# Optimization experiments

Measured on AMD Instinct MI355X. Metric: run time of the kernel, lower is better.

Reference implementation:

```python
import jax, jax.numpy as jnp
import numpy as np

HEADS = 8
DIM_HEAD = 64
SCALE = DIM_HEAD ** -0.5


def setup_inputs() -> dict:
    key = jax.random.key(0)
    k1, k2, k3 = jax.random.split(key, 3)
    B, N, D = 4, 2048, HEADS * DIM_HEAD  # D = inner_dim = 512
    x = jax.random.normal(k1, (B, N, D), dtype=jnp.float32)
    # nn.Linear weights stored transposed vs torch; here we use [in, out]
    w_qkv = jax.random.normal(k2, (D, 3 * D), dtype=jnp.float32) * (D ** -0.5)
    w_out = jax.random.normal(k3, (D, D), dtype=jnp.float32) * (D ** -0.5)
    b_out = jnp.zeros((D,), dtype=jnp.float32)
    return {"x": x, "w_qkv": w_qkv, "w_out": w_out, "b_out": b_out}


def reference(x, w_qkv, w_out, b_out):
    B, N, D = x.shape
    qkv = x @ w_qkv  # [B, N, 3D]
    q, k, v = jnp.split(qkv, 3, axis=-1)

    def to_heads(t):  # b n (h d) -> b h n d
        return t.reshape(B, N, HEADS, DIM_HEAD).transpose(0, 2, 1, 3)

    q, k, v = to_heads(q), to_heads(k), to_heads(v)
    dots = jnp.einsum('bhnd,bhmd->bhnm', q, k) * SCALE  # [B,H,N,N]
    attn = jax.nn.softmax(dots, axis=-1)
    out = jnp.einsum('bhnm,bhmd->bhnd', attn, v)  # [B,H,N,d]
    out = out.transpose(0, 2, 1, 3).reshape(B, N, D)  # b h n d -> b n (h d)
    return out @ w_out + b_out
```

## Files before the change

### kernel.cpp

```cpp
#include <hip/hip_runtime.h>

typedef __bf16 bf16;
typedef __bf16 bf16x8 __attribute__((ext_vector_type(8)));
typedef __bf16 bf16x4 __attribute__((ext_vector_type(4)));
typedef float f32x4 __attribute__((ext_vector_type(4)));
typedef float f32x16 __attribute__((ext_vector_type(16)));
typedef unsigned int uint2v __attribute__((ext_vector_type(2)));

#define MFMA16(a, b, c) __builtin_amdgcn_mfma_f32_16x16x32_bf16(a, b, c, 0, 0, 0)
#define MFMA32(a, b, c) __builtin_amdgcn_mfma_f32_32x32x16_bf16(a, b, c, 0, 0, 0)

#define CS 0.18033688011112042f

#if __has_builtin(__builtin_amdgcn_exp2f)
#define EXP2(x) __builtin_amdgcn_exp2f(x)
#else
#define EXP2(x) exp2f(x)
#endif

#define WAIT_VM0() __builtin_amdgcn_s_waitcnt(0x0F70)
#define WAIT_VM8() __builtin_amdgcn_s_waitcnt(0x0F78)

__device__ __forceinline__ void load_lds16(const bf16* g, bf16* l) {
    __builtin_amdgcn_global_load_lds(
        (const __attribute__((address_space(1))) unsigned int*)g,
        (__attribute__((address_space(3))) unsigned int*)l, 16, 0, 0);
}

#if __has_builtin(__builtin_amdgcn_permlane32_swap)
__device__ __forceinline__ bf16x8 build_bfrag(bf16x4 plo, bf16x4 phi, int ) {
    union { bf16x4 b; unsigned int i[2]; } ul, uh;
    ul.b = plo; uh.b = phi;
    uint2v r0 = __builtin_amdgcn_permlane32_swap(ul.i[0], uh.i[0], false, false);
    uint2v r1 = __builtin_amdgcn_permlane32_swap(ul.i[1], uh.i[1], false, false);
    union { unsigned int i[4]; bf16x8 b; } ub;
    ub.i[0] = r0[0]; ub.i[1] = r1[0]; ub.i[2] = r0[1]; ub.i[3] = r1[1];
    return ub.b;
}

__device__ __forceinline__ float sum_halves(float x) {
    union { float f; unsigned int u; } a; a.f = x;
    uint2v r = __builtin_amdgcn_permlane32_swap(a.u, a.u, false, false);
    union { unsigned int u; float f; } b0, b1;
    b0.u = r[0]; b1.u = r[1];
    return b0.f + b1.f;
}
#else
__device__ __forceinline__ bf16x4 shfl_xor32_b64(bf16x4 v) {
    union { bf16x4 b; int i[2]; } u;
    u.b = v;
    u.i[0] = __shfl_xor(u.i[0], 32, 64);
    u.i[1] = __shfl_xor(u.i[1], 32, 64);
    return u.b;
}
__device__ __forceinline__ bf16x8 build_bfrag(bf16x4 plo, bf16x4 phi, int h) {
    bf16x4 xlo = shfl_xor32_b64(plo);
    bf16x4 xhi = shfl_xor32_b64(phi);
    bf16x4 lo4 = h ? xhi : plo;
    bf16x4 hi4 = h ? phi : xlo;
    bf16x8 bb;
#pragma unroll
    for (int i = 0; i < 4; ++i) { bb[i] = lo4[i]; bb[4 + i] = hi4[i]; }
    return bb;
}
__device__ __forceinline__ float sum_halves(float x) {
    return x + __shfl_xor(x, 32, 64);
}
#endif

__global__ __launch_bounds__(256) void f32_to_bf16_kernel(const float* __restrict__ in,
                                                          bf16* __restrict__ out, int n) {
    int i = (blockIdx.x * 256 + threadIdx.x) * 4;
    if (i < n) {
        float4 v = *(const float4*)&in[i];
        bf16x4 o = {(bf16)v.x, (bf16)v.y, (bf16)v.z, (bf16)v.w};
        *(bf16x4*)&out[i] = o;
    }
}

__global__ __launch_bounds__(256) void transpose_f2b(const float* __restrict__ in,
                                                     bf16* __restrict__ out,
                                                     int R, int C) {
    __shared__ float tile[32][33];
    int tx = threadIdx.x & 31, ty = threadIdx.x >> 5;
    int c0 = blockIdx.x * 32, r0 = blockIdx.y * 32;
#pragma unroll
    for (int i = ty; i < 32; i += 8)
        tile[i][tx] = in[(size_t)(r0 + i) * C + c0 + tx];
    __syncthreads();
#pragma unroll
    for (int i = ty; i < 32; i += 8)
        out[(size_t)(c0 + i) * R + r0 + tx] = (bf16)tile[tx][i];
}

__global__ __launch_bounds__(256) void transpose_v_kernel(const bf16* __restrict__ qkv,
                                                          bf16* __restrict__ vt) {
    __shared__ bf16 tile[32][33];
    int tx = threadIdx.x & 31, ty = threadIdx.x >> 5;
    int bh = blockIdx.z, b = bh >> 3, h = bh & 7;
    int n0 = blockIdx.x * 32, d0 = blockIdx.y * 32;
#pragma unroll
    for (int i = ty; i < 32; i += 8)
        tile[i][tx] = qkv[(size_t)(b * 2048 + n0 + i) * 1536 + 1024 + h * 64 + d0 + tx];
    __syncthreads();
#pragma unroll
    for (int i = ty; i < 32; i += 8)
        vt[(size_t)(bh * 64 + d0 + i) * 2048 + n0 + tx] = tile[tx][i];
}

template <int MT, int MODE, typename OutT>
__global__ __launch_bounds__(256, (MT == 4) ? 2 : 4)
void gemm_bt_kernel(const bf16* __restrict__ A,
                    const bf16* __restrict__ Bt,
                    const float* __restrict__ bias,
                    OutT* __restrict__ C,
                    int M, int N, int K) {
    const int BM = MT * 32;
    __shared__ bf16 As[BM * 64];
    __shared__ bf16 Bs[128 * 64];
    int t = threadIdx.x;
    int lane = t & 63, w = t >> 6;
    int wr = w >> 1, wc = w & 1;
    int quad = lane >> 4, r16 = lane & 15;
    int m0 = blockIdx.y * BM, n0 = blockIdx.x * 128;

    const f32x4 fzero = {0.f, 0.f, 0.f, 0.f};
    f32x4 acc[MT][4];
#pragma unroll
    for (int i = 0; i < MT; ++i)
#pragma unroll
        for (int j = 0; j < 4; ++j) acc[i][j] = fzero;

    const bf16* ap[MT]; bf16* ad[MT];
    const bf16* bp[4];  bf16* bd[4];
#pragma unroll
    for (int i = 0; i < MT; ++i) {
        int ci = i * 256 + t;
        int row = ci >> 3, cp = ci & 7, cc = cp ^ (row & 7);
        ap[i] = &A[(size_t)(m0 + row) * K + cc * 8];
        ad[i] = &As[ci * 8];
    }
#pragma unroll
    for (int i = 0; i < 4; ++i) {
        int ci = i * 256 + t;
        int row = ci >> 3, cp = ci & 7, cc = cp ^ (row & 7);
        bp[i] = &Bt[(size_t)(n0 + row) * K + cc * 8];
        bd[i] = &Bs[ci * 8];
    }

    for (int k0 = 0; k0 < K; k0 += 64) {
        __syncthreads();
#pragma unroll
        for (int i = 0; i < MT; ++i) { load_lds16(ap[i], ad[i]); ap[i] += 64; }
#pragma unroll
        for (int i = 0; i < 4; ++i) { load_lds16(bp[i], bd[i]); bp[i] += 64; }
        __syncthreads();
#pragma unroll
        for (int ks = 0; ks < 2; ++ks) {
            bf16x8 af[MT], bfr[4];
            int cp = (ks * 4 + quad) ^ (r16 & 7);
#pragma unroll
            for (int mt = 0; mt < MT; ++mt)
                af[mt] = *(const bf16x8*)&As[(wr * (BM / 2) + mt * 16 + r16) * 64 + cp * 8];
#pragma unroll
            for (int nt = 0; nt < 4; ++nt)
                bfr[nt] = *(const bf16x8*)&Bs[(wc * 64 + nt * 16 + r16) * 64 + cp * 8];
#pragma unroll
            for (int mt = 0; mt < MT; ++mt)
#pragma unroll
                for (int nt = 0; nt < 4; ++nt)
                    acc[mt][nt] = MFMA16(af[mt], bfr[nt], acc[mt][nt]);
        }
    }
#pragma unroll
    for (int mt = 0; mt < MT; ++mt)
#pragma unroll
        for (int nt = 0; nt < 4; ++nt)
#pragma unroll
            for (int r = 0; r < 4; ++r) {
                int row = m0 + wr * (BM / 2) + mt * 16 + quad * 4 + r;
                int col = n0 + wc * 64 + nt * 16 + r16;
                float v = acc[mt][nt][r];
                if (MODE == 1 && n0 < 512) v *= CS;
                if (MODE == 2) v += bias[col];
                C[(size_t)row * N + col] = (OutT)v;
            }
}

__global__ __launch_bounds__(128, 2) void attn_kernel(const bf16* __restrict__ qkv,
                                                      const bf16* __restrict__ vt,
                                                      bf16* __restrict__ out) {
    __shared__ __align__(16) char smemraw[32768];
    bf16* stage = (bf16*)smemraw;

    int t = threadIdx.x;
    int lane = t & 63, w = t >> 6;
    int h = lane >> 5, q = lane & 31;
    int bh = blockIdx.y, b = bh >> 3, hd = bh & 7;
    int qb = blockIdx.x * 64;

    bf16x8 qf[2][4];
#pragma unroll
    for (int sub = 0; sub < 2; ++sub) {
        size_t qoff = (size_t)(b * 2048 + qb + sub * 32 + q) * 1536 + hd * 64;
#pragma unroll
        for (int s = 0; s < 4; ++s)
            qf[sub][s] = *(const bf16x8*)&qkv[qoff + s * 16 + h * 8];
    }

    f32x16 o_acc[2][2];
#pragma unroll
    for (int sub = 0; sub < 2; ++sub)
#pragma unroll
        for (int db = 0; db < 2; ++db)
#pragma unroll
            for (int i = 0; i < 16; ++i) o_acc[sub][db][i] = 0.f;
    float psum[2] = {0.f, 0.f};

    bf16* base = stage + w * 8192;

    const bf16* kp[4]; const bf16* vp[4];
    int kdo[4], vdo[4];
#pragma unroll
    for (int rdd = 0; rdd < 4; ++rdd) {
        int ciK = rdd * 64 + lane;
        int rowK = ciK >> 3, ccK = (ciK & 7) ^ (rowK & 7);
        kp[rdd] = &qkv[(size_t)(b * 2048 + w * 1024 + rowK) * 1536 + 512 + hd * 64 + ccK * 8];
        kdo[rdd] = ciK * 8;
        int ciV = rdd * 64 + lane;
        int rowV = ciV >> 2, ccV = (ciV & 3) ^ (rowV & 3);
        vp[rdd] = &vt[(size_t)(bh * 64 + rowV) * 2048 + w * 1024 + ccV * 8];
        vdo[rdd] = 2048 + ciV * 8;
    }

#pragma unroll
    for (int rdd = 0; rdd < 4; ++rdd) {
        load_lds16(kp[rdd], base + kdo[rdd]);  kp[rdd] += (size_t)32 * 1536;
        load_lds16(vp[rdd], base + vdo[rdd]);  vp[rdd] += 32;
    }

    for (int it = 0; it < 32; ++it) {
        const bf16* Ks = base + (it & 1) * 4096;
        const bf16* Vs = Ks + 2048;
        if (it < 31) {
            bf16* nb = base + ((it + 1) & 1) * 4096;
#pragma unroll
            for (int rdd = 0; rdd < 4; ++rdd) {
                load_lds16(kp[rdd], nb + kdo[rdd]);  kp[rdd] += (size_t)32 * 1536;
                load_lds16(vp[rdd], nb + vdo[rdd]);  vp[rdd] += 32;
            }
            WAIT_VM8();
        } else {
            WAIT_VM0();
        }

        bf16x8 kf[4];
#pragma unroll
        for (int s = 0; s < 4; ++s) {
            int cp = (s * 2 + h) ^ (q & 7);
            kf[s] = *(const bf16x8*)&Ks[q * 64 + cp * 8];
        }
        bf16x8 vf[2][2];
#pragma unroll
        for (int kstep = 0; kstep < 2; ++kstep)
#pragma unroll
            for (int db = 0; db < 2; ++db) {
                int cp = (kstep * 2 + h) ^ (q & 3);
                vf[kstep][db] = *(const bf16x8*)&Vs[(db * 32 + q) * 32 + cp * 8];
            }

#pragma unroll
        for (int sub = 0; sub < 2; ++sub) {
            f32x16 sacc;
#pragma unroll
            for (int i = 0; i < 16; ++i) sacc[i] = 0.f;
#pragma unroll
            for (int s = 0; s < 4; ++s)
                sacc = MFMA32(kf[s], qf[sub][s], sacc);

            bf16x4 pk[4];
            float ps0 = 0.f, ps1 = 0.f, ps2 = 0.f, ps3 = 0.f;
#pragma unroll
            for (int i = 0; i < 4; ++i) {
                float p0 = EXP2(sacc[i]);
                float p1 = EXP2(sacc[4 + i]);
                float p2 = EXP2(sacc[8 + i]);
                float p3 = EXP2(sacc[12 + i]);
                ps0 += p0; ps1 += p1; ps2 += p2; ps3 += p3;
                pk[0][i] = (bf16)p0; pk[1][i] = (bf16)p1;
                pk[2][i] = (bf16)p2; pk[3][i] = (bf16)p3;
            }
            psum[sub] += (ps0 + ps1) + (ps2 + ps3);
            bf16x8 bfr0 = build_bfrag(pk[0], pk[1], h);
            bf16x8 bfr1 = build_bfrag(pk[2], pk[3], h);

#pragma unroll
            for (int db = 0; db < 2; ++db) {
                o_acc[sub][db] = MFMA32(vf[0][db], bfr0, o_acc[sub][db]);
                o_acc[sub][db] = MFMA32(vf[1][db], bfr1, o_acc[sub][db]);
            }
        }
    }

    float l_own[2];
#pragma unroll
    for (int sub = 0; sub < 2; ++sub)
        l_own[sub] = sum_halves(psum[sub]);

    __syncthreads();
    float* Of = (float*)smemraw;
    float* Lf = (float*)(smemraw + 17408);

    if (w == 1) {
#pragma unroll
        for (int sub = 0; sub < 2; ++sub) {
#pragma unroll
            for (int db = 0; db < 2; ++db)
#pragma unroll
                for (int r = 0; r < 16; ++r) {
                    int d = db * 32 + (r & 3) + 8 * (r >> 2) + 4 * h;
                    Of[(sub * 32 + q) * 68 + d] = o_acc[sub][db][r];
                }
            if (h == 0) Lf[sub * 32 + q] = l_own[sub];
        }
    }
    __syncthreads();
    if (w == 0) {
#pragma unroll
        for (int sub = 0; sub < 2; ++sub) {
#pragma unroll
            for (int db = 0; db < 2; ++db)
#pragma unroll
                for (int r = 0; r < 16; ++r) {
                    int d = db * 32 + (r & 3) + 8 * (r >> 2) + 4 * h;
                    Of[(sub * 32 + q) * 68 + d] += o_acc[sub][db][r];
                }
            if (h == 0) Lf[sub * 32 + q] += l_own[sub];
        }
    }
    __syncthreads();

    {
        int row = t >> 1, half = t & 1;
        float linv = 1.f / Lf[row];
        const float* src = &Of[row * 68 + half * 32];
        bf16* dst = &out[(size_t)(b * 2048 + qb + row) * 512 + hd * 64 + half * 32];
#pragma unroll
        for (int i = 0; i < 4; ++i) {
            f32x4 a = *(const f32x4*)&src[i * 8];
            f32x4 c = *(const f32x4*)&src[i * 8 + 4];
            bf16x8 o8;
#pragma unroll
            for (int j = 0; j < 4; ++j) {
                o8[j] = (bf16)(a[j] * linv);
                o8[4 + j] = (bf16)(c[j] * linv);
            }
            *(bf16x8*)&dst[i * 8] = o8;
        }
    }
}

extern "C" void kernel_launch(void* const* d_in, const int* in_sizes, int n_in,
                              void* d_out, int out_size, void* d_ws, size_t ws_size,
                              hipStream_t stream) {
    const float* x     = (const float*)d_in[0];
    const float* w_qkv = (const float*)d_in[1];
    const float* w_out = (const float*)d_in[2];
    const float* b_out = (const float*)d_in[3];
    float* out = (float*)d_out;

    char* ws = (char*)d_ws;
    size_t off = 0;
    bf16* xb    = (bf16*)(ws + off); off += (size_t)8192 * 512 * 2;
    bf16* wqkvT = (bf16*)(ws + off); off += (size_t)1536 * 512 * 2;
    bf16* woutT = (bf16*)(ws + off); off += (size_t)512 * 512 * 2;
    bf16* qkv   = (bf16*)(ws + off); off += (size_t)8192 * 1536 * 2;
    bf16* vt    = (bf16*)(ws + off); off += (size_t)32 * 64 * 2048 * 2;
    bf16* attn  = (bf16*)(ws + off);

    f32_to_bf16_kernel<<<4096, 256, 0, stream>>>(x, xb, 8192 * 512);
    transpose_f2b<<<dim3(48, 16), 256, 0, stream>>>(w_qkv, wqkvT, 512, 1536);
    transpose_f2b<<<dim3(16, 16), 256, 0, stream>>>(w_out, woutT, 512, 512);
    gemm_bt_kernel<4, 1, bf16><<<dim3(12, 64), 256, 0, stream>>>(
        xb, wqkvT, nullptr, qkv, 8192, 1536, 512);
    transpose_v_kernel<<<dim3(64, 2, 32), 256, 0, stream>>>(qkv, vt);
    attn_kernel<<<dim3(32, 32), 128, 0, stream>>>(qkv, vt, attn);
    gemm_bt_kernel<2, 2, float><<<dim3(4, 128), 256, 0, stream>>>(
        attn, woutT, b_out, out, 8192, 512, 512);
}
```

Before: 164.4 us.

## Double-buffer GEMM LDS tiles and remap block indices for XCD locality

Double-buffers the GEMM shared-memory A/B tiles so the next K-slice's global-to-LDS loads are issued before computing the current slice. Waits use partial vmcnt counts with raw barriers. Both the GEMM and attention kernels remap linear block IDs so consecutive tiles land on the same XCD (stride-8 interleave), aiming for better L2 reuse. The extra LDS lowers the GEMM occupancy hint from 4 to 3 blocks for the smaller tile variant.

```diff
diff --git a/kernel.cpp b/kernel.cpp
--- a/kernel.cpp
+++ b/kernel.cpp
@@ -19,7 +19,11 @@
 #endif
 
 #define WAIT_VM0() __builtin_amdgcn_s_waitcnt(0x0F70)
+#define WAIT_VM6() __builtin_amdgcn_s_waitcnt(0x0F76)
 #define WAIT_VM8() __builtin_amdgcn_s_waitcnt(0x0F78)
+
+#define BARRIER() __builtin_amdgcn_s_barrier()
+#define CFENCE() asm volatile("" ::: "memory")
 
 __device__ __forceinline__ void load_lds16(const bf16* g, bf16* l) {
     __builtin_amdgcn_global_load_lds(
@@ -109,20 +113,26 @@
 }
 
 template <int MT, int MODE, typename OutT>
-__global__ __launch_bounds__(256, (MT == 4) ? 2 : 4)
+__global__ __launch_bounds__(256, (MT == 4) ? 2 : 3)
 void gemm_bt_kernel(const bf16* __restrict__ A,
                     const bf16* __restrict__ Bt,
                     const float* __restrict__ bias,
                     OutT* __restrict__ C,
                     int M, int N, int K) {
     const int BM = MT * 32;
-    __shared__ bf16 As[BM * 64];
-    __shared__ bf16 Bs[128 * 64];
+    const int ASZ = BM * 64, BSZ = 128 * 64;
+    __shared__ bf16 As[2 * ASZ];
+    __shared__ bf16 Bs[2 * BSZ];
     int t = threadIdx.x;
     int lane = t & 63, w = t >> 6;
     int wr = w >> 1, wc = w & 1;
     int quad = lane >> 4, r16 = lane & 15;
-    int m0 = blockIdx.y * BM, n0 = blockIdx.x * 128;
+
+    int lin = blockIdx.y * gridDim.x + blockIdx.x;
+    int cpx = (gridDim.x * gridDim.y) >> 3;
+    int nl = (lin & 7) * cpx + (lin >> 3);
+    int bx = nl % gridDim.x, by = nl / gridDim.x;
+    int m0 = by * BM, n0 = bx * 128;
 
     const f32x4 fzero = {0.f, 0.f, 0.f, 0.f};
     f32x4 acc[MT][4];
@@ -148,29 +158,43 @@
         bd[i] = &Bs[ci * 8];
     }
 
-    for (int k0 = 0; k0 < K; k0 += 64) {
-        __syncthreads();
-#pragma unroll
-        for (int i = 0; i < MT; ++i) { load_lds16(ap[i], ad[i]); ap[i] += 64; }
-#pragma unroll
-        for (int i = 0; i < 4; ++i) { load_lds16(bp[i], bd[i]); bp[i] += 64; }
-        __syncthreads();
+    auto stage = [&](int par) {
+#pragma unroll
+        for (int i = 0; i < MT; ++i) { load_lds16(ap[i], ad[i] + par * ASZ); ap[i] += 64; }
+#pragma unroll
+        for (int i = 0; i < 4; ++i) { load_lds16(bp[i], bd[i] + par * BSZ); bp[i] += 64; }
+    };
+
+    stage(0);
+    int nk = K >> 6;
+    for (int kk = 0; kk < nk; ++kk) {
+        if (kk + 1 < nk) {
+            stage((kk + 1) & 1);
+            if constexpr (MT == 4) WAIT_VM8(); else WAIT_VM6();
+        } else {
+            WAIT_VM0();
+        }
+        CFENCE(); BARRIER(); CFENCE();
+
+        const bf16* Asb = &As[(kk & 1) * ASZ];
+        const bf16* Bsb = &Bs[(kk & 1) * BSZ];
 #pragma unroll
         for (int ks = 0; ks < 2; ++ks) {
             bf16x8 af[MT], bfr[4];
             int cp = (ks * 4 + quad) ^ (r16 & 7);
 #pragma unroll
             for (int mt = 0; mt < MT; ++mt)
-                af[mt] = *(const bf16x8*)&As[(wr * (BM / 2) + mt * 16 + r16) * 64 + cp * 8];
+                af[mt] = *(const bf16x8*)&Asb[(wr * (BM / 2) + mt * 16 + r16) * 64 + cp * 8];
 #pragma unroll
             for (int nt = 0; nt < 4; ++nt)
-                bfr[nt] = *(const bf16x8*)&Bs[(wc * 64 + nt * 16 + r16) * 64 + cp * 8];
+                bfr[nt] = *(const bf16x8*)&Bsb[(wc * 64 + nt * 16 + r16) * 64 + cp * 8];
 #pragma unroll
             for (int mt = 0; mt < MT; ++mt)
 #pragma unroll
                 for (int nt = 0; nt < 4; ++nt)
                     acc[mt][nt] = MFMA16(af[mt], bfr[nt], acc[mt][nt]);
         }
+        if (kk + 1 < nk) { CFENCE(); BARRIER(); CFENCE(); }
     }
 #pragma unroll
     for (int mt = 0; mt < MT; ++mt)
@@ -196,8 +220,11 @@
     int t = threadIdx.x;
     int lane = t & 63, w = t >> 6;
     int h = lane >> 5, q = lane & 31;
-    int bh = blockIdx.y, b = bh >> 3, hd = bh & 7;
-    int qb = blockIdx.x * 64;
+
+    int lin = blockIdx.y * gridDim.x + blockIdx.x;
+    int nl = (lin & 7) * 128 + (lin >> 3);
+    int bh = nl >> 5, b = bh >> 3, hd = bh & 7;
+    int qb = (nl & 31) * 64;
 
     bf16x8 qf[2][4];
 #pragma unroll
```

Measured after the change: 167.1 us. No clear change (+1.6%).
